# Performance work log

Measured on AMD Instinct MI355X. Metric: run time of the kernel, lower is better.

The kernel has to match this reference:

```python
import jax, jax.numpy as jnp
import numpy as np

EPS = 1e-5
HEADS = 4
RES = 28          # resolution H = W
PS = 14           # patch_size (pooled grid side)
POOL = RES // PS  # patch_pool_size = 2


def _local_init_pos_w():
    # Deterministic local init (locality_strength=1.0); kernel_size = sqrt(num_heads) = 2
    ks = int(HEADS ** 0.5)
    center = (ks - 1) / 2 if ks % 2 == 0 else ks // 2
    w = np.zeros((HEADS, 3), dtype=np.float32)
    for h1 in range(ks):
        for h2 in range(ks):
            pos = h1 + ks * h2
            w[pos, 2] = -1.0
            w[pos, 1] = 2.0 * (h1 - center)
            w[pos, 0] = 2.0 * (h2 - center)
    return jnp.asarray(w)


def setup_inputs() -> dict:
    key = jax.random.key(0)
    B, T, C = 32, RES * RES, 768
    x = jax.random.normal(key, (B, T, C), dtype=jnp.float32)
    return {
        "x": x,
        "weight": jnp.ones((C,), jnp.float32),
        "bias": jnp.zeros((C,), jnp.float32),
        "mean_norm_weight": jnp.zeros((HEADS,), jnp.float32),
        "var_norm_weight": jnp.zeros((HEADS,), jnp.float32),
        "pos_w": _local_init_pos_w(),
        "pos_b": jnp.zeros((HEADS,), jnp.float32),
    }


def _rel_indices(ps, dtype):
    # (P, P, 3) relative position features: [indx, indy, indx^2 + indy^2]
    ind = jnp.arange(ps)[None, :] - jnp.arange(ps)[:, None]  # (ps, ps)
    indx = jnp.tile(ind, (ps, ps))                            # (P, P)
    indy = jnp.repeat(jnp.repeat(ind, ps, axis=0), ps, axis=1)
    return jnp.stack([indx, indy, indx * indx + indy * indy], axis=-1).astype(dtype)


def reference(x, weight, bias, mean_norm_weight, var_norm_weight, pos_w, pos_b):
    B, T, C = x.shape
    Ch = C // HEADS
    P = PS * PS

    # group "moment2" normalization
    g = x.reshape(B, T, HEADS, Ch)
    m2 = jnp.mean(g * g, axis=3, keepdims=True)
    xn = (g / jnp.sqrt(m2 + EPS)).reshape(B, T, C)

    mw = jax.nn.sigmoid(mean_norm_weight)  # (HEADS,)
    vw = jax.nn.sigmoid(var_norm_weight)

    # position scores: Linear(3 -> heads) then softmax over source-patch axis
    rel = _rel_indices(PS, x.dtype)                 # (P, P, 3)
    scores = rel @ pos_w.T + pos_b                  # (P, P, HEADS)
    pos = jax.nn.softmax(scores, axis=0)            # softmax over dim -2 of (B,h,i,j)
    pos_h = jnp.transpose(pos, (2, 0, 1))           # (HEADS, P, P)

    mean_ln = xn.mean(axis=2)                       # (B, T)
    var_ln = xn.var(axis=2, ddof=1)                 # torch unbiased var

    # spatialize + avg-pool POOLxPOOL
    xs = xn.reshape(B, RES, RES, C).transpose(0, 3, 1, 2)          # (B, C, 28, 28)
    xp = xs.reshape(B, C, PS, POOL, PS, POOL).mean(axis=(3, 5))    # (B, C, 14, 14)
    xp = xp.reshape(B, HEADS, Ch, P)

    mean_r = jnp.einsum('bhci,hij->bhcj', xp, pos_h)
    mean2_r = jnp.einsum('bhci,hij->bhcj', xp * xp, pos_h)
    var_r = mean2_r - mean_r * mean_r

    def unpool(y):  # nearest-neighbor upsample back to T tokens
        y = y.reshape(B, HEADS, Ch, PS, PS)
        y = jnp.broadcast_to(y[:, :, :, :, None, :, None],
                             (B, HEADS, Ch, PS, POOL, PS, POOL))
        return y.reshape(B, HEADS, Ch, T)

    mean_r = unpool(mean_r)
    var_r = unpool(var_r)

    mwv = mw.reshape(1, HEADS, 1, 1)
    vwv = vw.reshape(1, HEADS, 1, 1)
    mean_r = (1.0 - mwv) * mean_r + mwv * mean_ln[:, None, None, :]
    var_r = (1.0 - vwv) * var_r + vwv * var_ln[:, None, None, :]

    mean_r = mean_r.reshape(B, C, T).transpose(0, 2, 1)  # (B, T, C)
    var_r = var_r.reshape(B, C, T).transpose(0, 2, 1)

    out = (xn - mean_r) / jnp.sqrt(var_r + EPS)
    return out * weight.reshape(1, 1, C) + bias.reshape(1, 1, C)
```

## Files before the change

### kernel.cpp

```cpp
#include <hip/hip_runtime.h>

#define NB   32
#define NT   784
#define NC   768
#define NH   4
#define CH   192
#define PSZ  14
#define NP   196
#define RESO 28
#define EPSV 1e-5f

__global__ __launch_bounds__(64) void k_pos(
    const float* __restrict__ pos_w, const float* __restrict__ pos_b,
    const float* __restrict__ mnw,   const float* __restrict__ vnw,
    float* __restrict__ fn, float* __restrict__ gn, float* __restrict__ mwvw) {
  int t = threadIdx.x;
  if (t < 8) {
    float v = (t < 4) ? mnw[t] : vnw[t - 4];
    mwvw[t] = 1.f / (1.f + expf(-v));
  }
  if (t < NH * PSZ) {
    int h = t / PSZ, j = t % PSZ;
    float w0 = pos_w[h * 3 + 0];
    float w1 = pos_w[h * 3 + 1];
    float w2 = pos_w[h * 3 + 2];
    float e[PSZ];

    float mx = -1e30f;
#pragma unroll
    for (int i = 0; i < PSZ; ++i) {
      float d = (float)(j - i);
      float s = w0 * d + w2 * d * d;
      e[i] = s;
      mx = fmaxf(mx, s);
    }
    float sum = 0.f;
#pragma unroll
    for (int i = 0; i < PSZ; ++i) { e[i] = expf(e[i] - mx); sum += e[i]; }
    float inv = 1.f / sum;
#pragma unroll
    for (int i = 0; i < PSZ; ++i) fn[(h * PSZ + j) * PSZ + i] = e[i] * inv;

    mx = -1e30f;
#pragma unroll
    for (int i = 0; i < PSZ; ++i) {
      float d = (float)(j - i);
      float s = w1 * d + w2 * d * d;
      e[i] = s;
      mx = fmaxf(mx, s);
    }
    sum = 0.f;
#pragma unroll
    for (int i = 0; i < PSZ; ++i) { e[i] = expf(e[i] - mx); sum += e[i]; }
    inv = 1.f / sum;
#pragma unroll
    for (int i = 0; i < PSZ; ++i) gn[(h * PSZ + j) * PSZ + i] = e[i] * inv;
  }
}

__global__ __launch_bounds__(256) void k_norm_pool(
    const float* __restrict__ x,
    float* __restrict__ inv_m2, float* __restrict__ mean_ln,
    float* __restrict__ var_ln, float4* __restrict__ xp4) {
  __shared__ float4 xl4[4 * 192];
  int bid = blockIdx.x;
  int b = bid / NP, ip = bid % NP;
  int pr = ip / PSZ, pc = ip % PSZ;
  int tid = threadIdx.x;
  int k = tid >> 6, lane = tid & 63;
  int t = (2 * pr + (k >> 1)) * RESO + (2 * pc + (k & 1));

  const float4* row = (const float4*)(x + (size_t)(b * NT + t) * NC);
  float4 v0 = row[lane], v1 = row[lane + 64], v2 = row[lane + 128];
  int h0 = lane / 48;
  int h1 = (lane + 64) / 48;
  int h2 = (lane + 128) / 48;

  float d0 = v0.x * v0.x + v0.y * v0.y + v0.z * v0.z + v0.w * v0.w;
  float d1 = v1.x * v1.x + v1.y * v1.y + v1.z * v1.z + v1.w * v1.w;
  float d2 = v2.x * v2.x + v2.y * v2.y + v2.z * v2.z + v2.w * v2.w;
  float s0 = (h0 == 0) ? d0 : 0.f;
  float s1 = ((h0 == 1) ? d0 : 0.f) + ((h1 == 1) ? d1 : 0.f);
  float s2 = ((h1 == 2) ? d1 : 0.f) + ((h2 == 2) ? d2 : 0.f);
  float s3 = (h2 == 3) ? d2 : 0.f;
#pragma unroll
  for (int d = 32; d >= 1; d >>= 1) {
    s0 += __shfl_xor(s0, d, 64);
    s1 += __shfl_xor(s1, d, 64);
    s2 += __shfl_xor(s2, d, 64);
    s3 += __shfl_xor(s3, d, 64);
  }
  float i0 = rsqrtf(s0 * (1.f / CH) + EPSV);
  float i1 = rsqrtf(s1 * (1.f / CH) + EPSV);
  float i2 = rsqrtf(s2 * (1.f / CH) + EPSV);
  float i3 = rsqrtf(s3 * (1.f / CH) + EPSV);
  if (lane < 4) {
    float iv = (lane == 0) ? i0 : (lane == 1) ? i1 : (lane == 2) ? i2 : i3;
    inv_m2[(size_t)(b * NT + t) * NH + lane] = iv;
  }

  float f0 = (h0 == 0) ? i0 : i1;
  float f1 = (h1 == 1) ? i1 : i2;
  float f2 = (h2 == 2) ? i2 : i3;
  v0.x *= f0; v0.y *= f0; v0.z *= f0; v0.w *= f0;
  v1.x *= f1; v1.y *= f1; v1.z *= f1; v1.w *= f1;
  v2.x *= f2; v2.y *= f2; v2.z *= f2; v2.w *= f2;

  float sm = v0.x + v0.y + v0.z + v0.w + v1.x + v1.y + v1.z + v1.w +
             v2.x + v2.y + v2.z + v2.w;
  float sq = v0.x * v0.x + v0.y * v0.y + v0.z * v0.z + v0.w * v0.w +
             v1.x * v1.x + v1.y * v1.y + v1.z * v1.z + v1.w * v1.w +
             v2.x * v2.x + v2.y * v2.y + v2.z * v2.z + v2.w * v2.w;
#pragma unroll
  for (int d = 32; d >= 1; d >>= 1) {
    sm += __shfl_xor(sm, d, 64);
    sq += __shfl_xor(sq, d, 64);
  }
  if (lane == 0) {
    float mean = sm / (float)NC;
    mean_ln[b * NT + t] = mean;
    var_ln[b * NT + t] = (sq - (float)NC * mean * mean) / (float)(NC - 1);
  }

  xl4[k * 192 + lane] = v0;
  xl4[k * 192 + lane + 64] = v1;
  xl4[k * 192 + lane + 128] = v2;
  __syncthreads();

  if (tid < 192) {
    float4 a = xl4[tid], bb = xl4[192 + tid], c = xl4[384 + tid], d = xl4[576 + tid];
    float4 r;
    r.x = (a.x + bb.x + c.x + d.x) * 0.25f;
    r.y = (a.y + bb.y + c.y + d.y) * 0.25f;
    r.z = (a.z + bb.z + c.z + d.z) * 0.25f;
    r.w = (a.w + bb.w + c.w + d.w) * 0.25f;
    xp4[(size_t)(b * NP + ip) * 192 + tid] = r;
  }
}

__global__ __launch_bounds__(256) void k_fused(
    const float* __restrict__ xp, const float* __restrict__ fn,
    const float* __restrict__ gn, const float* __restrict__ x,
    const float* __restrict__ weight, const float* __restrict__ bias,
    const float* __restrict__ inv_m2, const float* __restrict__ mean_ln,
    const float* __restrict__ var_ln, const float* __restrict__ mwvw,
    float* __restrict__ out) {
  __shared__ float fns[NH * PSZ];
  __shared__ float gns[NH * PSZ * PSZ];
  __shared__ float tstat[4 * PSZ][6];

  int bid = blockIdx.x;
  int b = bid / PSZ, jx = bid % PSZ;
  int tid = threadIdx.x;
  int h = tid >> 6, lane = tid & 63;
  int c0 = h * CH + lane, c1 = c0 + 64, c2 = c0 + 128;

  if (tid < NH * PSZ) {
    int hh = tid / PSZ, ix = tid % PSZ;
    fns[tid] = fn[(hh * PSZ + jx) * PSZ + ix];
  }
  for (int i = tid; i < NH * PSZ * PSZ; i += 256) gns[i] = gn[i];
  for (int idx = tid; idx < 4 * PSZ * 6; idx += 256) {
    int l = idx / 6, f = idx % 6;
    int jy = l >> 2, kk = l & 3;
    int t = (2 * jy + (kk >> 1)) * RESO + (2 * jx + (kk & 1));
    size_t o = (size_t)(b * NT + t);
    tstat[l][f] = (f < 4) ? inv_m2[o * NH + f]
                : (f == 4) ? mean_ln[o] : var_ln[o];
  }
  __syncthreads();

  float t1[PSZ][3], t2[PSZ][3];
#pragma unroll
  for (int iy = 0; iy < PSZ; ++iy)
#pragma unroll
    for (int k = 0; k < 3; ++k) { t1[iy][k] = 0.f; t2[iy][k] = 0.f; }

  const float* base = xp + (size_t)b * NP * NC;
#pragma unroll
  for (int iy = 0; iy < PSZ; ++iy) {
    const float* prow = base + (size_t)iy * PSZ * NC;
#pragma unroll
    for (int ix = 0; ix < PSZ; ++ix) {
      float f = fns[h * PSZ + ix];
      const float* row = prow + ix * NC;
      float v0 = row[c0], v1 = row[c1], v2 = row[c2];
      t1[iy][0] += f * v0; t2[iy][0] += f * (v0 * v0);
      t1[iy][1] += f * v1; t2[iy][1] += f * (v1 * v1);
      t1[iy][2] += f * v2; t2[iy][2] += f * (v2 * v2);
    }
  }

  float wv0 = weight[c0], wv1 = weight[c1], wv2 = weight[c2];
  float bv0 = bias[c0],   bv1 = bias[c1],   bv2 = bias[c2];
  float mw = mwvw[h], vw = mwvw[4 + h];
  float omw = 1.f - mw, ovw = 1.f - vw;
  const float* gh = &gns[h * NP];

#pragma unroll 1
  for (int jy = 0; jy < PSZ; ++jy) {
    float m0 = 0.f, m1 = 0.f, m2v = 0.f, q0 = 0.f, q1 = 0.f, q2 = 0.f;
#pragma unroll
    for (int iy = 0; iy < PSZ; ++iy) {
      float g = gh[jy * PSZ + iy];
      m0  += g * t1[iy][0]; q0 += g * t2[iy][0];
      m1  += g * t1[iy][1]; q1 += g * t2[iy][1];
      m2v += g * t1[iy][2]; q2 += g * t2[iy][2];
    }
    float p0 = fmaxf(q0 - m0 * m0, 0.f);
    float p1 = fmaxf(q1 - m1 * m1, 0.f);
    float p2 = fmaxf(q2 - m2v * m2v, 0.f);
    float mb0 = omw * m0, mb1 = omw * m1, mb2 = omw * m2v;
    float vb0 = ovw * p0, vb1 = ovw * p1, vb2 = ovw * p2;

#pragma unroll
    for (int kk = 0; kk < 4; ++kk) {
      int t = (2 * jy + (kk >> 1)) * RESO + (2 * jx + (kk & 1));
      size_t xo = (size_t)(b * NT + t) * NC;
      int l = jy * 4 + kk;
      float iv = tstat[l][h];
      float ml = tstat[l][4], vl = tstat[l][5];

      float xn0 = x[xo + c0] * iv;
      float xn1 = x[xo + c1] * iv;
      float xn2 = x[xo + c2] * iv;

      float mr0 = mb0 + mw * ml;
      float mr1 = mb1 + mw * ml;
      float mr2 = mb2 + mw * ml;
      float vr0 = vb0 + vw * vl;
      float vr1 = vb1 + vw * vl;
      float vr2 = vb2 + vw * vl;

      out[xo + c0] = (xn0 - mr0) * rsqrtf(vr0 + EPSV) * wv0 + bv0;
      out[xo + c1] = (xn1 - mr1) * rsqrtf(vr1 + EPSV) * wv1 + bv1;
      out[xo + c2] = (xn2 - mr2) * rsqrtf(vr2 + EPSV) * wv2 + bv2;
    }
  }
}

extern "C" void kernel_launch(void* const* d_in, const int* in_sizes, int n_in,
                              void* d_out, int out_size, void* d_ws, size_t ws_size,
                              hipStream_t stream) {
  const float* x     = (const float*)d_in[0];
  const float* wgt   = (const float*)d_in[1];
  const float* bias  = (const float*)d_in[2];
  const float* mnw   = (const float*)d_in[3];
  const float* vnw   = (const float*)d_in[4];
  const float* pos_w = (const float*)d_in[5];
  const float* pos_b = (const float*)d_in[6];
  float* out = (float*)d_out;

  float* ws      = (float*)d_ws;
  float* fn      = ws;
  float* gn      = fn + NH * PSZ * PSZ;
  float* mwvw    = gn + NH * PSZ * PSZ;
  float* inv_m2  = mwvw + 8;
  float* mean_ln = inv_m2 + (size_t)NB * NT * NH;
  float* var_ln  = mean_ln + (size_t)NB * NT;
  float* xp      = var_ln + (size_t)NB * NT;

  hipLaunchKernelGGL(k_pos, dim3(1), dim3(64), 0, stream,
                     pos_w, pos_b, mnw, vnw, fn, gn, mwvw);
  hipLaunchKernelGGL(k_norm_pool, dim3(NB * NP), dim3(256), 0, stream,
                     x, inv_m2, mean_ln, var_ln, (float4*)xp);
  hipLaunchKernelGGL(k_fused, dim3(NB * PSZ), dim3(256), 0, stream,
                     xp, fn, gn, x, wgt, bias, inv_m2, mean_ln, var_ln, mwvw, out);
}
```

Before: 181.8 us.

## Fuse positional softmax into main kernel, split channels across 3x blocks, remap norm lanes

Removes the separate single-block positional-softmax kernel and recomputes the softmax tables and sigmoid gates inside each block of the fused kernel. The fused kernel now gives each thread one channel instead of three and launches three times as many blocks. Block indices are swizzled across groups of 8. In the norm/pool kernel, each 16-lane group now owns one head's contiguous channels, so the per-head sum of squares needs a 16-lane reduction instead of four 64-lane reductions. The aim is to cut launch overhead, register pressure and shuffle work and to raise occupancy. In exchange, every block redundantly computes the softmax tables, and the float4 loads are strided by 3, which hurts coalescing. pos_b is dropped, which is only correct because a constant bias cancels inside the softmax.

New measurement: 177.3 us. 2.5% less time.

```diff
diff --git a/kernel.cpp b/kernel.cpp
--- a/kernel.cpp
+++ b/kernel.cpp
@@ -9,54 +9,6 @@
 #define NP   196
 #define RESO 28
 #define EPSV 1e-5f
-
-__global__ __launch_bounds__(64) void k_pos(
-    const float* __restrict__ pos_w, const float* __restrict__ pos_b,
-    const float* __restrict__ mnw,   const float* __restrict__ vnw,
-    float* __restrict__ fn, float* __restrict__ gn, float* __restrict__ mwvw) {
-  int t = threadIdx.x;
-  if (t < 8) {
-    float v = (t < 4) ? mnw[t] : vnw[t - 4];
-    mwvw[t] = 1.f / (1.f + expf(-v));
-  }
-  if (t < NH * PSZ) {
-    int h = t / PSZ, j = t % PSZ;
-    float w0 = pos_w[h * 3 + 0];
-    float w1 = pos_w[h * 3 + 1];
-    float w2 = pos_w[h * 3 + 2];
-    float e[PSZ];
-
-    float mx = -1e30f;
-#pragma unroll
-    for (int i = 0; i < PSZ; ++i) {
-      float d = (float)(j - i);
-      float s = w0 * d + w2 * d * d;
-      e[i] = s;
-      mx = fmaxf(mx, s);
-    }
-    float sum = 0.f;
-#pragma unroll
-    for (int i = 0; i < PSZ; ++i) { e[i] = expf(e[i] - mx); sum += e[i]; }
-    float inv = 1.f / sum;
-#pragma unroll
-    for (int i = 0; i < PSZ; ++i) fn[(h * PSZ + j) * PSZ + i] = e[i] * inv;
-
-    mx = -1e30f;
-#pragma unroll
-    for (int i = 0; i < PSZ; ++i) {
-      float d = (float)(j - i);
-      float s = w1 * d + w2 * d * d;
-      e[i] = s;
-      mx = fmaxf(mx, s);
-    }
-    sum = 0.f;
-#pragma unroll
-    for (int i = 0; i < PSZ; ++i) { e[i] = expf(e[i] - mx); sum += e[i]; }
-    inv = 1.f / sum;
-#pragma unroll
-    for (int i = 0; i < PSZ; ++i) gn[(h * PSZ + j) * PSZ + i] = e[i] * inv;
-  }
-}
 
 __global__ __launch_bounds__(256) void k_norm_pool(
     const float* __restrict__ x,
@@ -71,40 +23,21 @@
   int t = (2 * pr + (k >> 1)) * RESO + (2 * pc + (k & 1));
 
   const float4* row = (const float4*)(x + (size_t)(b * NT + t) * NC);
-  float4 v0 = row[lane], v1 = row[lane + 64], v2 = row[lane + 128];
-  int h0 = lane / 48;
-  int h1 = (lane + 64) / 48;
-  int h2 = (lane + 128) / 48;
-
-  float d0 = v0.x * v0.x + v0.y * v0.y + v0.z * v0.z + v0.w * v0.w;
-  float d1 = v1.x * v1.x + v1.y * v1.y + v1.z * v1.z + v1.w * v1.w;
-  float d2 = v2.x * v2.x + v2.y * v2.y + v2.z * v2.z + v2.w * v2.w;
-  float s0 = (h0 == 0) ? d0 : 0.f;
-  float s1 = ((h0 == 1) ? d0 : 0.f) + ((h1 == 1) ? d1 : 0.f);
-  float s2 = ((h1 == 2) ? d1 : 0.f) + ((h2 == 2) ? d2 : 0.f);
-  float s3 = (h2 == 3) ? d2 : 0.f;
-#pragma unroll
-  for (int d = 32; d >= 1; d >>= 1) {
-    s0 += __shfl_xor(s0, d, 64);
-    s1 += __shfl_xor(s1, d, 64);
-    s2 += __shfl_xor(s2, d, 64);
-    s3 += __shfl_xor(s3, d, 64);
-  }
-  float i0 = rsqrtf(s0 * (1.f / CH) + EPSV);
-  float i1 = rsqrtf(s1 * (1.f / CH) + EPSV);
-  float i2 = rsqrtf(s2 * (1.f / CH) + EPSV);
-  float i3 = rsqrtf(s3 * (1.f / CH) + EPSV);
-  if (lane < 4) {
-    float iv = (lane == 0) ? i0 : (lane == 1) ? i1 : (lane == 2) ? i2 : i3;
-    inv_m2[(size_t)(b * NT + t) * NH + lane] = iv;
-  }
-
-  float f0 = (h0 == 0) ? i0 : i1;
-  float f1 = (h1 == 1) ? i1 : i2;
-  float f2 = (h2 == 2) ? i2 : i3;
-  v0.x *= f0; v0.y *= f0; v0.z *= f0; v0.w *= f0;
-  v1.x *= f1; v1.y *= f1; v1.z *= f1; v1.w *= f1;
-  v2.x *= f2; v2.y *= f2; v2.z *= f2; v2.w *= f2;
+  int f4b = (lane >> 4) * 48 + (lane & 15) * 3;
+  float4 v0 = row[f4b], v1 = row[f4b + 1], v2 = row[f4b + 2];
+
+  float d = v0.x * v0.x + v0.y * v0.y + v0.z * v0.z + v0.w * v0.w +
+            v1.x * v1.x + v1.y * v1.y + v1.z * v1.z + v1.w * v1.w +
+            v2.x * v2.x + v2.y * v2.y + v2.z * v2.z + v2.w * v2.w;
+#pragma unroll
+  for (int s = 1; s <= 8; s <<= 1) d += __shfl_xor(d, s, 64);
+  float iv = rsqrtf(d * (1.f / CH) + EPSV);
+  if ((lane & 15) == 0)
+    inv_m2[(size_t)(b * NT + t) * NH + (lane >> 4)] = iv;
+
+  v0.x *= iv; v0.y *= iv; v0.z *= iv; v0.w *= iv;
+  v1.x *= iv; v1.y *= iv; v1.z *= iv; v1.w *= iv;
+  v2.x *= iv; v2.y *= iv; v2.z *= iv; v2.w *= iv;
 
   float sm = v0.x + v0.y + v0.z + v0.w + v1.x + v1.y + v1.z + v1.w +
              v2.x + v2.y + v2.z + v2.w;
@@ -112,9 +45,9 @@
              v1.x * v1.x + v1.y * v1.y + v1.z * v1.z + v1.w * v1.w +
              v2.x * v2.x + v2.y * v2.y + v2.z * v2.z + v2.w * v2.w;
 #pragma unroll
-  for (int d = 32; d >= 1; d >>= 1) {
-    sm += __shfl_xor(sm, d, 64);
-    sq += __shfl_xor(sq, d, 64);
+  for (int s = 1; s <= 32; s <<= 1) {
+    sm += __shfl_xor(sm, s, 64);
+    sq += __shfl_xor(sq, s, 64);
   }
   if (lane == 0) {
     float mean = sm / (float)NC;
@@ -122,44 +55,81 @@
     var_ln[b * NT + t] = (sq - (float)NC * mean * mean) / (float)(NC - 1);
   }
 
-  xl4[k * 192 + lane] = v0;
-  xl4[k * 192 + lane + 64] = v1;
-  xl4[k * 192 + lane + 128] = v2;
+  xl4[k * 192 + f4b]     = v0;
+  xl4[k * 192 + f4b + 1] = v1;
+  xl4[k * 192 + f4b + 2] = v2;
   __syncthreads();
 
   if (tid < 192) {
-    float4 a = xl4[tid], bb = xl4[192 + tid], c = xl4[384 + tid], d = xl4[576 + tid];
+    float4 a = xl4[tid], bb = xl4[192 + tid], c = xl4[384 + tid], dd = xl4[576 + tid];
     float4 r;
-    r.x = (a.x + bb.x + c.x + d.x) * 0.25f;
-    r.y = (a.y + bb.y + c.y + d.y) * 0.25f;
-    r.z = (a.z + bb.z + c.z + d.z) * 0.25f;
-    r.w = (a.w + bb.w + c.w + d.w) * 0.25f;
+    r.x = (a.x + bb.x + c.x + dd.x) * 0.25f;
+    r.y = (a.y + bb.y + c.y + dd.y) * 0.25f;
+    r.z = (a.z + bb.z + c.z + dd.z) * 0.25f;
+    r.w = (a.w + bb.w + c.w + dd.w) * 0.25f;
     xp4[(size_t)(b * NP + ip) * 192 + tid] = r;
   }
 }
 
 __global__ __launch_bounds__(256) void k_fused(
-    const float* __restrict__ xp, const float* __restrict__ fn,
-    const float* __restrict__ gn, const float* __restrict__ x,
+    const float* __restrict__ xp, const float* __restrict__ pos_w,
+    const float* __restrict__ mnw, const float* __restrict__ vnw,
+    const float* __restrict__ x,
     const float* __restrict__ weight, const float* __restrict__ bias,
     const float* __restrict__ inv_m2, const float* __restrict__ mean_ln,
-    const float* __restrict__ var_ln, const float* __restrict__ mwvw,
-    float* __restrict__ out) {
+    const float* __restrict__ var_ln, float* __restrict__ out) {
   __shared__ float fns[NH * PSZ];
   __shared__ float gns[NH * PSZ * PSZ];
   __shared__ float tstat[4 * PSZ][6];
-
-  int bid = blockIdx.x;
-  int b = bid / PSZ, jx = bid % PSZ;
+  __shared__ float sgate[8];
+
+  int bid0 = blockIdx.x;
+  int bid = (bid0 & 7) * 168 + (bid0 >> 3);
+  int b = bid / 42, r = bid % 42;
+  int s = r / PSZ, jx = r % PSZ;
   int tid = threadIdx.x;
   int h = tid >> 6, lane = tid & 63;
-  int c0 = h * CH + lane, c1 = c0 + 64, c2 = c0 + 128;
+  int c = h * CH + s * 64 + lane;
 
   if (tid < NH * PSZ) {
-    int hh = tid / PSZ, ix = tid % PSZ;
-    fns[tid] = fn[(hh * PSZ + jx) * PSZ + ix];
-  }
-  for (int i = tid; i < NH * PSZ * PSZ; i += 256) gns[i] = gn[i];
+    int hh = tid / PSZ, jr = tid % PSZ;
+    float w1 = pos_w[hh * 3 + 1], w2 = pos_w[hh * 3 + 2];
+    float e[PSZ], mx = -1e30f;
+#pragma unroll
+    for (int i = 0; i < PSZ; ++i) {
+      float dd = (float)(jr - i);
+      float sc = w1 * dd + w2 * dd * dd;
+      e[i] = sc; mx = fmaxf(mx, sc);
+    }
+    float sum = 0.f;
+#pragma unroll
+    for (int i = 0; i < PSZ; ++i) { e[i] = expf(e[i] - mx); sum += e[i]; }
+    float invs = 1.f / sum;
+#pragma unroll
+    for (int i = 0; i < PSZ; ++i) gns[(hh * PSZ + jr) * PSZ + i] = e[i] * invs;
+  }
+  if (tid >= 64 && tid < 64 + NH) {
+    int hh = tid - 64;
+    float w0 = pos_w[hh * 3 + 0], w2 = pos_w[hh * 3 + 2];
+    float e[PSZ], mx = -1e30f;
+#pragma unroll
+    for (int i = 0; i < PSZ; ++i) {
+      float dd = (float)(jx - i);
+      float sc = w0 * dd + w2 * dd * dd;
+      e[i] = sc; mx = fmaxf(mx, sc);
+    }
+    float sum = 0.f;
+#pragma unroll
+    for (int i = 0; i < PSZ; ++i) { e[i] = expf(e[i] - mx); sum += e[i]; }
+    float invs = 1.f / sum;
+#pragma unroll
+    for (int i = 0; i < PSZ; ++i) fns[hh * PSZ + i] = e[i] * invs;
+  }
+  if (tid >= 72 && tid < 80) {
+    int g = tid - 72;
+    float v = (g < 4) ? mnw[g] : vnw[g - 4];
+    sgate[g] = 1.f / (1.f + expf(-v));
+  }
   for (int idx = tid; idx < 4 * PSZ * 6; idx += 256) {
     int l = idx / 6, f = idx % 6;
     int jy = l >> 2, kk = l & 3;
@@ -170,71 +140,52 @@
   }
   __syncthreads();
 
-  float t1[PSZ][3], t2[PSZ][3];
-#pragma unroll
-  for (int iy = 0; iy < PSZ; ++iy)
-#pragma unroll
-    for (int k = 0; k < 3; ++k) { t1[iy][k] = 0.f; t2[iy][k] = 0.f; }
-
-  const float* base = xp + (size_t)b * NP * NC;
+  float t1[PSZ], t2[PSZ];
+#pragma unroll
+  for (int iy = 0; iy < PSZ; ++iy) { t1[iy] = 0.f; t2[iy] = 0.f; }
+
+  const float* base = xp + (size_t)b * NP * NC + c;
 #pragma unroll
   for (int iy = 0; iy < PSZ; ++iy) {
-    const float* prow = base + (size_t)iy * PSZ * NC;
+    const float* prow = base + (size_t)(iy * PSZ) * NC;
 #pragma unroll
     for (int ix = 0; ix < PSZ; ++ix) {
       float f = fns[h * PSZ + ix];
-      const float* row = prow + ix * NC;
-      float v0 = row[c0], v1 = row[c1], v2 = row[c2];
-      t1[iy][0] += f * v0; t2[iy][0] += f * (v0 * v0);
-      t1[iy][1] += f * v1; t2[iy][1] += f * (v1 * v1);
-      t1[iy][2] += f * v2; t2[iy][2] += f * (v2 * v2);
-    }
-  }
-
-  float wv0 = weight[c0], wv1 = weight[c1], wv2 = weight[c2];
-  float bv0 = bias[c0],   bv1 = bias[c1],   bv2 = bias[c2];
-  float mw = mwvw[h], vw = mwvw[4 + h];
+      float v = prow[ix * NC];
+      t1[iy] += f * v;
+      t2[iy] += f * (v * v);
+    }
+  }
+
+  float wv = weight[c], bv = bias[c];
+  float mw = sgate[h], vw = sgate[4 + h];
   float omw = 1.f - mw, ovw = 1.f - vw;
   const float* gh = &gns[h * NP];
 
 #pragma unroll 1
   for (int jy = 0; jy < PSZ; ++jy) {
-    float m0 = 0.f, m1 = 0.f, m2v = 0.f, q0 = 0.f, q1 = 0.f, q2 = 0.f;
+    float m = 0.f, q = 0.f;
 #pragma unroll
     for (int iy = 0; iy < PSZ; ++iy) {
       float g = gh[jy * PSZ + iy];
-      m0  += g * t1[iy][0]; q0 += g * t2[iy][0];
-      m1  += g * t1[iy][1]; q1 += g * t2[iy][1];
-      m2v += g * t1[iy][2]; q2 += g * t2[iy][2];
-    }
-    float p0 = fmaxf(q0 - m0 * m0, 0.f);
-    float p1 = fmaxf(q1 - m1 * m1, 0.f);
-    float p2 = fmaxf(q2 - m2v * m2v, 0.f);
-    float mb0 = omw * m0, mb1 = omw * m1, mb2 = omw * m2v;
-    float vb0 = ovw * p0, vb1 = ovw * p1, vb2 = ovw * p2;
+      m += g * t1[iy];
+      q += g * t2[iy];
+    }
+    float p = fmaxf(q - m * m, 0.f);
+    float mb = omw * m, vb = ovw * p;
 
 #pragma unroll
     for (int kk = 0; kk < 4; ++kk) {
       int t = (2 * jy + (kk >> 1)) * RESO + (2 * jx + (kk & 1));
       size_t xo = (size_t)(b * NT + t) * NC;
       int l = jy * 4 + kk;
-      float iv = tstat[l][h];
+      float ivv = tstat[l][h];
       float ml = tstat[l][4], vl = tstat[l][5];
 
-      float xn0 = x[xo + c0] * iv;
-      float xn1 = x[xo + c1] * iv;
-      float xn2 = x[xo + c2] * iv;
-
-      float mr0 = mb0 + mw * ml;
-      float mr1 = mb1 + mw * ml;
-      float mr2 = mb2 + mw * ml;
-      float vr0 = vb0 + vw * vl;
-      float vr1 = vb1 + vw * vl;
-      float vr2 = vb2 + vw * vl;
-
-      out[xo + c0] = (xn0 - mr0) * rsqrtf(vr0 + EPSV) * wv0 + bv0;
-      out[xo + c1] = (xn1 - mr1) * rsqrtf(vr1 + EPSV) * wv1 + bv1;
-      out[xo + c2] = (xn2 - mr2) * rsqrtf(vr2 + EPSV) * wv2 + bv2;
+      float xn = x[xo + c] * ivv;
+      float mr = mb + mw * ml;
+      float vr = vb + vw * vl;
+      out[xo + c] = (xn - mr) * rsqrtf(vr + EPSV) * wv + bv;
     }
   }
 }
@@ -248,22 +199,16 @@
   const float* mnw   = (const float*)d_in[3];
   const float* vnw   = (const float*)d_in[4];
   const float* pos_w = (const float*)d_in[5];
-  const float* pos_b = (const float*)d_in[6];
   float* out = (float*)d_out;
 
   float* ws      = (float*)d_ws;
-  float* fn      = ws;
-  float* gn      = fn + NH * PSZ * PSZ;
-  float* mwvw    = gn + NH * PSZ * PSZ;
-  float* inv_m2  = mwvw + 8;
+  float* inv_m2  = ws;
   float* mean_ln = inv_m2 + (size_t)NB * NT * NH;
   float* var_ln  = mean_ln + (size_t)NB * NT;
   float* xp      = var_ln + (size_t)NB * NT;
 
-  hipLaunchKernelGGL(k_pos, dim3(1), dim3(64), 0, stream,
-                     pos_w, pos_b, mnw, vnw, fn, gn, mwvw);
   hipLaunchKernelGGL(k_norm_pool, dim3(NB * NP), dim3(256), 0, stream,
                      x, inv_m2, mean_ln, var_ln, (float4*)xp);
-  hipLaunchKernelGGL(k_fused, dim3(NB * PSZ), dim3(256), 0, stream,
-                     xp, fn, gn, x, wgt, bias, inv_m2, mean_ln, var_ln, mwvw, out);
+  hipLaunchKernelGGL(k_fused, dim3(NB * 3 * PSZ), dim3(256), 0, stream,
+                     xp, pos_w, mnw, vnw, x, wgt, bias, inv_m2, mean_ln, var_ln, out);
 }
```
